# Optimization experiments

Measured on AMD Instinct MI355X. Metric: run time of the kernel, lower is better.

The kernel has to match this reference:

```python
import jax, jax.numpy as jnp
import numpy as np

ALPHA = 0.1

def grad_f(p):
    # analytic gradient of f(p) = sum(p**2)
    return 2.0 * p

def setup_inputs() -> dict:
    key = jax.random.key(0)
    p = jax.random.normal(key, (16384, 64), dtype=jnp.float32)
    return {"p": p}

def reference(p):
    # p: [N, D]
    g = grad_f(p)                                   # [N, D]
    scores = jnp.einsum('id,jd->ij', g, g)          # torch.inner(g, g) -> [N, N]
    w = jax.nn.softmax(-scores, axis=-1)            # [N, N]
    # einsum('ijd,ij->id', p[None,:,:]-p[:,None,:], w)
    #   = w @ p - sum_j(w[i,j]) * p[i]   (avoids the NxNxD intermediate)
    agg = jnp.matmul(w, p) - jnp.sum(w, axis=-1, keepdims=True) * p  # [N, D]
    return p + agg * ALPHA
```

## Files before the change

kernel.cpp:

```cpp
#include <hip/hip_runtime.h>
#include <stdint.h>

#define NROWS 16384
#define DIM 64
#define BK 64
#define NT (NROWS / BK)
#define NQB (NROWS / 128)
#define TILE_BYTES 16384
#define VT_OFF 8192
#define LOG2E 1.4426950408889634f
#define MHAT_COEF 20.0f

typedef __attribute__((ext_vector_type(8))) _Float16 f16x8;
typedef __attribute__((ext_vector_type(8))) unsigned short ushort8;
typedef __attribute__((ext_vector_type(4))) float f32x4;
typedef __attribute__((ext_vector_type(8))) __bf16 bf16x8;
typedef __attribute__((ext_vector_type(8))) short short8;

static __device__ __forceinline__ f32x4 mfma_f16(f16x8 a, f16x8 b, f32x4 c) {
  return __builtin_amdgcn_mfma_f32_16x16x32_f16(a, b, c, 0, 0, 0);
}
static __device__ __forceinline__ f32x4 mfma_bf16(short8 a, short8 b, f32x4 c) {
  return __builtin_amdgcn_mfma_f32_16x16x32_bf16(
      __builtin_bit_cast(bf16x8, a), __builtin_bit_cast(bf16x8, b), c, 0, 0, 0);
}
static __device__ __forceinline__ void gload_lds16(const void* g, void* l) {
  __builtin_amdgcn_global_load_lds(
      (const __attribute__((address_space(1))) unsigned int*)(uintptr_t)g,
      (__attribute__((address_space(3))) unsigned int*)(unsigned int)(uintptr_t)l,
      16, 0, 0);
}
static __device__ __forceinline__ float fast_exp2(float x) {
  return __builtin_amdgcn_exp2f(x);
}
static __device__ __forceinline__ unsigned short f2bfbits(float x) {
  return __builtin_bit_cast(unsigned short, (__bf16)x);
}
static __device__ __forceinline__ unsigned short f2bf(float x) {
  unsigned u = __builtin_bit_cast(unsigned, x);
  u = (u + 0x7fffu + ((u >> 16) & 1u)) >> 16;
  return (unsigned short)u;
}
static __device__ __forceinline__ float bf2f(unsigned short b) {
  return __builtin_bit_cast(float, ((unsigned)b) << 16);
}

__global__ __launch_bounds__(256)
void pack_kernel(const float* __restrict__ p, unsigned char* __restrict__ tiles,
                 float* __restrict__ mhat) {
  __shared__ unsigned short sT[64][68];
  const int kt = blockIdx.x;
  const int t  = threadIdx.x;
  const int r  = t >> 2;
  const int q4 = t & 3;
  const int d0 = q4 * 16;

  const float* src = p + ((size_t)(kt * 64 + r)) * DIM + d0;
  float4 f0 = ((const float4*)src)[0];
  float4 f1 = ((const float4*)src)[1];
  float4 f2 = ((const float4*)src)[2];
  float4 f3 = ((const float4*)src)[3];
  float v[16] = {f0.x, f0.y, f0.z, f0.w, f1.x, f1.y, f1.z, f1.w,
                 f2.x, f2.y, f2.z, f2.w, f3.x, f3.y, f3.z, f3.w};
  ushort8 h0, h1, hb0, hb1;
  float sq = 0.f;
#pragma unroll
  for (int i = 0; i < 8; ++i) {
    h0[i]  = __builtin_bit_cast(unsigned short, (_Float16)v[i]);
    h1[i]  = __builtin_bit_cast(unsigned short, (_Float16)v[8 + i]);
    hb0[i] = f2bf(v[i]);
    hb1[i] = f2bf(v[8 + i]);
    sq = fmaf(v[i], v[i], sq);
    sq = fmaf(v[8 + i], v[8 + i], sq);
  }
  unsigned char* tb = tiles + (size_t)kt * TILE_BYTES;
  const int swz = (r & 7) << 4;
  *(ushort8*)(tb + r * 128 + ((2 * d0) ^ swz))      = h0;
  *(ushort8*)(tb + r * 128 + ((2 * d0 + 16) ^ swz)) = h1;

  sq += __shfl_xor(sq, 1);
  sq += __shfl_xor(sq, 2);
  if (q4 == 0) mhat[kt * 64 + r] = MHAT_COEF * LOG2E * sqrtf(sq);

  *(ushort8*)&sT[r][d0]     = hb0;
  *(ushort8*)&sT[r][d0 + 8] = hb1;
  __syncthreads();
  const int d    = t >> 2;
  const int base = (q4 >> 1) * 32 + (q4 & 1) * 8;
  ushort8 a8, b8;
#pragma unroll
  for (int j = 0; j < 8; ++j) {
    a8[j] = sT[base + (j >> 2) * 16 + (j & 3)][d];
    b8[j] = sT[base + (j >> 2) * 16 + 4 + (j & 3)][d];
  }
  const int swzd = (d & 7) << 4;
  *(ushort8*)(tb + VT_OFF + d * 128 + ((2 * (q4 * 16)) ^ swzd))      = a8;
  *(ushort8*)(tb + VT_OFF + d * 128 + ((2 * (q4 * 16) + 16) ^ swzd)) = b8;
}

__global__ __launch_bounds__(256)
void attn_main(const float* __restrict__ p, const unsigned char* __restrict__ tiles,
               const float* __restrict__ mhat, float* __restrict__ out,
               float* __restrict__ partO, float* __restrict__ partL,
               int S, int writeDirect) {
  __shared__ __align__(16) unsigned char sbuf[2][TILE_BYTES];

  const int t  = threadIdx.x;
  const int w  = t >> 6;
  const int l  = t & 63;
  const int lr = l & 15;
  const int lg = l >> 4;
  const int qt = blockIdx.x;
  const int s  = blockIdx.y;
  const int ntp = NT / S;
  const int kt0 = s * ntp;
  const int swz = (lr & 7) << 4;
  const int ko0 = (lg * 16) ^ swz;
  const int ko1 = (64 + lg * 16) ^ swz;

  f16x8 qf[2][2];
  float nm[2];
#pragma unroll
  for (int g = 0; g < 2; ++g) {
    const int grow = w * 32 + g * 16;
    const unsigned char* qtb =
        tiles + (size_t)(qt * 2 + (grow >> 6)) * TILE_BYTES;
    const int rin = (grow & 63) + lr;
    qf[g][0] = *(const f16x8*)(qtb + rin * 128 + ko0);
    qf[g][1] = *(const f16x8*)(qtb + rin * 128 + ko1);
    nm[g] = -mhat[qt * 128 + grow + lr];
  }

  const f32x4 z4 = {0.f, 0.f, 0.f, 0.f};
  f32x4 oacc[2][4] = {{z4, z4, z4, z4}, {z4, z4, z4, z4}};
  float lrun[2] = {0.f, 0.f};
  const float S2 = -4.0f * LOG2E;

  auto STAGE = [&](int kt, int b) {
    const unsigned char* g = tiles + (size_t)kt * TILE_BYTES + (w * 4) * 1024 + l * 16;
    unsigned char* lb = &sbuf[b][(w * 4) * 1024];
#pragma unroll
    for (int c = 0; c < 4; ++c)
      gload_lds16(g + c * 1024, lb + c * 1024);
  };

  STAGE(kt0, 0);
  __syncthreads();

  for (int i = 0; i < ntp; ++i) {
    if (i + 1 < ntp) STAGE(kt0 + i + 1, (i + 1) & 1);

    const unsigned char* kb = &sbuf[i & 1][0];

    f32x4 acc[2][4] = {{z4, z4, z4, z4}, {z4, z4, z4, z4}};
#pragma unroll
    for (int c = 0; c < 4; ++c) {
      f16x8 kf0 = *(const f16x8*)(kb + (c * 16 + lr) * 128 + ko0);
      f16x8 kf1 = *(const f16x8*)(kb + (c * 16 + lr) * 128 + ko1);
      acc[0][c] = mfma_f16(kf0, qf[0][0], acc[0][c]);
      acc[1][c] = mfma_f16(kf0, qf[1][0], acc[1][c]);
      acc[0][c] = mfma_f16(kf1, qf[0][1], acc[0][c]);
      acc[1][c] = mfma_f16(kf1, qf[1][1], acc[1][c]);
    }

    short8 pb[2][2];
#pragma unroll
    for (int g = 0; g < 2; ++g) {
      float pe[4][4];
#pragma unroll
      for (int c = 0; c < 4; ++c) {
#pragma unroll
        for (int r = 0; r < 4; ++r)
          pe[c][r] = fast_exp2(fmaf(acc[g][c][r], S2, nm[g]));
        lrun[g] += (pe[c][0] + pe[c][1]) + (pe[c][2] + pe[c][3]);
      }
#pragma unroll
      for (int r = 0; r < 4; ++r) {
        pb[g][0][r]     = (short)f2bfbits(pe[0][r]);
        pb[g][0][4 + r] = (short)f2bfbits(pe[1][r]);
        pb[g][1][r]     = (short)f2bfbits(pe[2][r]);
        pb[g][1][4 + r] = (short)f2bfbits(pe[3][r]);
      }
    }

#pragma unroll
    for (int kc = 0; kc < 2; ++kc) {
      const int ko = kc ? ko1 : ko0;
#pragma unroll
      for (int dc = 0; dc < 4; ++dc) {
        short8 vb = *(const short8*)(kb + VT_OFF + (dc * 16 + lr) * 128 + ko);
        oacc[0][dc] = mfma_bf16(pb[0][kc], vb, oacc[0][dc]);
        oacc[1][dc] = mfma_bf16(pb[1][kc], vb, oacc[1][dc]);
      }
    }

    __syncthreads();
  }

#pragma unroll
  for (int g = 0; g < 2; ++g) {
    float lsum = lrun[g];
    lsum += __shfl_xor(lsum, 16);
    lsum += __shfl_xor(lsum, 32);

    if (writeDirect) {
      float lq[4];
#pragma unroll
      for (int r = 0; r < 4; ++r) lq[r] = __shfl(lsum, lg * 4 + r);
#pragma unroll
      for (int r = 0; r < 4; ++r) {
        const float inv = 1.0f / lq[r];
        const size_t grow = (size_t)(qt * 128 + w * 32 + g * 16 + lg * 4 + r) * DIM;
#pragma unroll
        for (int dc = 0; dc < 4; ++dc) {
          const int col = dc * 16 + lr;
          const float pv = p[grow + col];
          out[grow + col] = pv + 0.1f * (oacc[g][dc][r] * inv - pv);
        }
      }
    } else {
      float* po = partO + (size_t)(qt * S + s) * 8192;
      float* pl = partL + (size_t)(qt * S + s) * 128;
#pragma unroll
      for (int r = 0; r < 4; ++r) {
        const int row = w * 32 + g * 16 + lg * 4 + r;
#pragma unroll
        for (int dc = 0; dc < 4; ++dc)
          po[row * 64 + dc * 16 + lr] = oacc[g][dc][r];
      }
      if (l < 16) pl[w * 32 + g * 16 + l] = lsum;
    }
  }
}

__global__ __launch_bounds__(256)
void reduce_kernel(const float* __restrict__ p, const float* __restrict__ partO,
                   const float* __restrict__ partL, float* __restrict__ out, int S) {
  const int t   = threadIdx.x;
  const int row = blockIdx.x * 16 + (t >> 4);
  const int c0  = (t & 15) * 4;
  const int qt  = row >> 7;
  const int rin = row & 127;

  float L = 0.f;
  float4 O = {0.f, 0.f, 0.f, 0.f};
  for (int s2 = 0; s2 < S; ++s2) {
    const size_t b = (size_t)(qt * S + s2);
    L += partL[b * 128 + rin];
    const float4 o4 = *(const float4*)&partO[b * 8192 + rin * 64 + c0];
    O.x += o4.x; O.y += o4.y; O.z += o4.z; O.w += o4.w;
  }
  const float inv = 1.0f / L;
  const float4 pv = *(const float4*)&p[(size_t)row * DIM + c0];
  float4 r;
  r.x = pv.x + 0.1f * (O.x * inv - pv.x);
  r.y = pv.y + 0.1f * (O.y * inv - pv.y);
  r.z = pv.z + 0.1f * (O.z * inv - pv.z);
  r.w = pv.w + 0.1f * (O.w * inv - pv.w);
  *(float4*)&out[(size_t)row * DIM + c0] = r;
}

#define LDE 88
__global__ __launch_bounds__(256)
void grad_attn_fb(const float* __restrict__ p, float* __restrict__ out) {
  __shared__ __align__(16) unsigned short sKhi[BK][LDE];
  __shared__ __align__(16) unsigned short sKlo[BK][LDE];
  __shared__ __align__(16) unsigned short sVt[DIM][LDE];
  __shared__ __align__(16) unsigned short sP[4][16][LDE];
  const int t = threadIdx.x, w = t >> 6, l = t & 63, lr = l & 15, lg = l >> 4;
  const int q0 = blockIdx.x * 64 + w * 16;
  short8 qhi[2], qlo[2];
#pragma unroll
  for (int kc = 0; kc < 2; ++kc) {
    const float* qp = p + (size_t)(q0 + lr) * DIM + kc * 32 + lg * 8;
    float4 fa = *(const float4*)qp;
    float4 fb = *(const float4*)(qp + 4);
    float v[8] = {fa.x, fa.y, fa.z, fa.w, fb.x, fb.y, fb.z, fb.w};
    short8 h, lo2;
#pragma unroll
    for (int i = 0; i < 8; ++i) {
      unsigned short hb = f2bf(v[i]);
      h[i] = (short)hb;
      lo2[i] = (short)f2bf(v[i] - bf2f(hb));
    }
    qhi[kc] = h; qlo[kc] = lo2;
  }
  const f32x4 z4 = {0.f, 0.f, 0.f, 0.f};
  f32x4 oacc[4] = {z4, z4, z4, z4};
  float mrun[4] = {-1e30f, -1e30f, -1e30f, -1e30f};
  float lrun[4] = {0.f, 0.f, 0.f, 0.f};
  const int srow = (t >> 3) * 2, sc0 = (t & 7) * 8;
  const int scs = sc0 ^ (((srow >> 3) & 7) << 3);
  const float S2 = -4.0f * LOG2E;
  for (int kt = 0; kt < NT; ++kt) {
    const int kv0 = kt * BK;
    __syncthreads();
    {
      const float* s0 = p + (size_t)(kv0 + srow) * DIM + sc0;
      float4 a0 = *(const float4*)s0;
      float4 b0 = *(const float4*)(s0 + 4);
      float4 a1 = *(const float4*)(s0 + DIM);
      float4 b1 = *(const float4*)(s0 + DIM + 4);
      float v0[8] = {a0.x, a0.y, a0.z, a0.w, b0.x, b0.y, b0.z, b0.w};
      float v1[8] = {a1.x, a1.y, a1.z, a1.w, b1.x, b1.y, b1.z, b1.w};
      short8 h0, h1, l0, l1;
#pragma unroll
      for (int i = 0; i < 8; ++i) {
        unsigned short hb0 = f2bf(v0[i]);
        unsigned short hb1 = f2bf(v1[i]);
        h0[i] = (short)hb0; l0[i] = (short)f2bf(v0[i] - bf2f(hb0));
        h1[i] = (short)hb1; l1[i] = (short)f2bf(v1[i] - bf2f(hb1));
      }
      *(short8*)&sKhi[srow][scs] = h0;
      *(short8*)&sKlo[srow][scs] = l0;
      *(short8*)&sKhi[srow + 1][scs] = h1;
      *(short8*)&sKlo[srow + 1][scs] = l1;
#pragma unroll
      for (int i = 0; i < 8; ++i) {
        int d = sc0 + i;
        unsigned pk = (unsigned)(unsigned short)h0[i] |
                      (((unsigned)(unsigned short)h1[i]) << 16);
        *(unsigned*)&sVt[d][srow ^ (((d >> 3) & 7) << 3)] = pk;
      }
    }
    __syncthreads();
    f32x4 acc[4] = {z4, z4, z4, z4};
#pragma unroll
    for (int c = 0; c < 4; ++c) {
      const int krow = c * 16 + lr;
      const int swc = ((krow >> 3) & 7) << 3;
#pragma unroll
      for (int kc = 0; kc < 2; ++kc) {
        const int off = (kc * 32 + lg * 8) ^ swc;
        short8 bh = *(const short8*)&sKhi[krow][off];
        short8 bl = *(const short8*)&sKlo[krow][off];
        acc[c] = mfma_bf16(qhi[kc], bh, acc[c]);
        acc[c] = mfma_bf16(qhi[kc], bl, acc[c]);
        acc[c] = mfma_bf16(qlo[kc], bh, acc[c]);
      }
    }
    float P[4][4];
#pragma unroll
    for (int r = 0; r < 4; ++r) {
      float e0 = acc[0][r] * S2, e1 = acc[1][r] * S2;
      float e2 = acc[2][r] * S2, e3 = acc[3][r] * S2;
      float mt = fmaxf(fmaxf(e0, e1), fmaxf(e2, e3));
      mt = fmaxf(mt, __shfl_xor(mt, 1));
      mt = fmaxf(mt, __shfl_xor(mt, 2));
      mt = fmaxf(mt, __shfl_xor(mt, 4));
      mt = fmaxf(mt, __shfl_xor(mt, 8));
      const float mn = fmaxf(mrun[r], mt);
      const float sc = exp2f(mrun[r] - mn);
      mrun[r] = mn;
      float p0 = exp2f(e0 - mn), p1 = exp2f(e1 - mn);
      float p2 = exp2f(e2 - mn), p3 = exp2f(e3 - mn);
      P[0][r] = p0; P[1][r] = p1; P[2][r] = p2; P[3][r] = p3;
      float ps = (p0 + p1) + (p2 + p3);
      ps += __shfl_xor(ps, 1);
      ps += __shfl_xor(ps, 2);
      ps += __shfl_xor(ps, 4);
      ps += __shfl_xor(ps, 8);
      lrun[r] = lrun[r] * sc + ps;
#pragma unroll
      for (int dc = 0; dc < 4; ++dc) oacc[dc][r] *= sc;
    }
    {
      const int irow = lg * 4;
      const int swp = ((l >> 5) & 1) << 3;
#pragma unroll
      for (int c = 0; c < 4; ++c) {
        const int colb = (c * 16 + lr) ^ swp;
#pragma unroll
        for (int r = 0; r < 4; ++r) sP[w][irow + r][colb] = f2bf(P[c][r]);
      }
    }
#pragma unroll
    for (int kc = 0; kc < 2; ++kc) {
      const int kb = kc * 32 + lg * 8;
      short8 pa = *(const short8*)&sP[w][lr][kb ^ (((lr >> 3) & 1) << 3)];
#pragma unroll
      for (int dc = 0; dc < 4; ++dc) {
        const int d = dc * 16 + lr;
        short8 vb = *(const short8*)&sVt[d][kb ^ (((d >> 3) & 7) << 3)];
        oacc[dc] = mfma_bf16(pa, vb, oacc[dc]);
      }
    }
  }
#pragma unroll
  for (int r = 0; r < 4; ++r) {
    const float inv = 1.0f / lrun[r];
    const size_t grow = (size_t)(q0 + lg * 4 + r) * DIM;
#pragma unroll
    for (int dc = 0; dc < 4; ++dc) {
      const int col = dc * 16 + lr;
      const float pv = p[grow + col];
      out[grow + col] = pv + 0.1f * (oacc[dc][r] * inv - pv);
    }
  }
}

extern "C" void kernel_launch(void* const* d_in, const int* in_sizes, int n_in,
                              void* d_out, int out_size, void* d_ws, size_t ws_size,
                              hipStream_t stream) {
  const float* p = (const float*)d_in[0];
  float* out = (float*)d_out;
  unsigned char* ws = (unsigned char*)d_ws;
  const size_t tiles_bytes = (size_t)NT * TILE_BYTES;
  const size_t mhat_bytes  = (size_t)NROWS * sizeof(float);
  const size_t base = tiles_bytes + mhat_bytes;

  if (ws_size < base) {
    grad_attn_fb<<<dim3(NROWS / 64), dim3(256), 0, stream>>>(p, out);
    return;
  }
  int S = 16;
  while (S > 1) {
    size_t need = base + (size_t)NQB * S * (8192 + 128) * sizeof(float);
    if (need <= ws_size) break;
    S >>= 1;
  }
  float* mhat  = (float*)(ws + tiles_bytes);
  float* partO = (float*)(ws + base);
  float* partL = partO + (size_t)NQB * S * 8192;

  pack_kernel<<<dim3(NT), dim3(256), 0, stream>>>(p, ws, mhat);
  attn_main<<<dim3(NQB, S), dim3(256), 0, stream>>>(p, ws, mhat, out, partO, partL,
                                                    S, S == 1 ? 1 : 0);
  if (S > 1)
    reduce_kernel<<<dim3(NROWS / 16), dim3(256), 0, stream>>>(p, partO, partL, out, S);
}
```

Baseline: 97.40 us.

## Split waves across query and key halves with LDS cross-wave reduction

The four waves are repartitioned from 4 query groups of 32 rows into 2 query groups of 64 rows times 2 key halves. Each wave now holds 64 query rows and processes 32 keys per tile. K and V fragments loaded from LDS are therefore reused across 4 query sub-blocks instead of 2, which halves LDS fragment reads per MFMA. At the end the two key-half waves combine their output accumulators and row sums through shared memory before the epilogue. This costs more registers (oacc grows to 4x4) and adds an extra sync plus an LDS reduction, and only half the waves do the final writes.

```diff
diff --git a/kernel.cpp b/kernel.cpp
--- a/kernel.cpp
+++ b/kernel.cpp
@@ -104,36 +104,42 @@
                float* __restrict__ partO, float* __restrict__ partL,
                int S, int writeDirect) {
   __shared__ __align__(16) unsigned char sbuf[2][TILE_BYTES];
-
-  const int t  = threadIdx.x;
-  const int w  = t >> 6;
-  const int l  = t & 63;
-  const int lr = l & 15;
-  const int lg = l >> 4;
-  const int qt = blockIdx.x;
-  const int s  = blockIdx.y;
+  __shared__ float sL[2][4][64];
+
+  const int t   = threadIdx.x;
+  const int w   = t >> 6;
+  const int l   = t & 63;
+  const int lr  = l & 15;
+  const int lg  = l >> 4;
+  const int wq  = w >> 1;
+  const int wkv = w & 1;
+  const int qt  = blockIdx.x;
+  const int s   = blockIdx.y;
   const int ntp = NT / S;
   const int kt0 = s * ntp;
   const int swz = (lr & 7) << 4;
   const int ko0 = (lg * 16) ^ swz;
   const int ko1 = (64 + lg * 16) ^ swz;
-
-  f16x8 qf[2][2];
-  float nm[2];
-#pragma unroll
-  for (int g = 0; g < 2; ++g) {
-    const int grow = w * 32 + g * 16;
-    const unsigned char* qtb =
-        tiles + (size_t)(qt * 2 + (grow >> 6)) * TILE_BYTES;
-    const int rin = (grow & 63) + lr;
+  const int kopv = (wkv * 64 + lg * 16) ^ swz;
+
+  const unsigned char* qtb = tiles + (size_t)(qt * 2 + wq) * TILE_BYTES;
+  f16x8 qf[4][2];
+  float nm[4];
+#pragma unroll
+  for (int g = 0; g < 4; ++g) {
+    const int rin = g * 16 + lr;
     qf[g][0] = *(const f16x8*)(qtb + rin * 128 + ko0);
     qf[g][1] = *(const f16x8*)(qtb + rin * 128 + ko1);
-    nm[g] = -mhat[qt * 128 + grow + lr];
+    nm[g] = -mhat[qt * 128 + wq * 64 + g * 16 + lr];
   }
 
   const f32x4 z4 = {0.f, 0.f, 0.f, 0.f};
-  f32x4 oacc[2][4] = {{z4, z4, z4, z4}, {z4, z4, z4, z4}};
-  float lrun[2] = {0.f, 0.f};
+  f32x4 oacc[4][4];
+#pragma unroll
+  for (int g = 0; g < 4; ++g)
+#pragma unroll
+    for (int dc = 0; dc < 4; ++dc) oacc[g][dc] = z4;
+  float lrun[4] = {0.f, 0.f, 0.f, 0.f};
   const float S2 = -4.0f * LOG2E;
 
   auto STAGE = [&](int kt, int b) {
@@ -152,83 +158,107 @@
 
     const unsigned char* kb = &sbuf[i & 1][0];
 
-    f32x4 acc[2][4] = {{z4, z4, z4, z4}, {z4, z4, z4, z4}};
-#pragma unroll
-    for (int c = 0; c < 4; ++c) {
-      f16x8 kf0 = *(const f16x8*)(kb + (c * 16 + lr) * 128 + ko0);
-      f16x8 kf1 = *(const f16x8*)(kb + (c * 16 + lr) * 128 + ko1);
-      acc[0][c] = mfma_f16(kf0, qf[0][0], acc[0][c]);
-      acc[1][c] = mfma_f16(kf0, qf[1][0], acc[1][c]);
-      acc[0][c] = mfma_f16(kf1, qf[0][1], acc[0][c]);
-      acc[1][c] = mfma_f16(kf1, qf[1][1], acc[1][c]);
-    }
-
-    short8 pb[2][2];
-#pragma unroll
-    for (int g = 0; g < 2; ++g) {
-      float pe[4][4];
-#pragma unroll
-      for (int c = 0; c < 4; ++c) {
-#pragma unroll
-        for (int r = 0; r < 4; ++r)
-          pe[c][r] = fast_exp2(fmaf(acc[g][c][r], S2, nm[g]));
-        lrun[g] += (pe[c][0] + pe[c][1]) + (pe[c][2] + pe[c][3]);
-      }
+    f32x4 acc[4][2];
+#pragma unroll
+    for (int g = 0; g < 4; ++g) { acc[g][0] = z4; acc[g][1] = z4; }
+#pragma unroll
+    for (int c = 0; c < 2; ++c) {
+      const int krow = (wkv * 32 + c * 16 + lr) * 128;
+      f16x8 kf0 = *(const f16x8*)(kb + krow + ko0);
+      f16x8 kf1 = *(const f16x8*)(kb + krow + ko1);
+#pragma unroll
+      for (int g = 0; g < 4; ++g) {
+        acc[g][c] = mfma_f16(kf0, qf[g][0], acc[g][c]);
+        acc[g][c] = mfma_f16(kf1, qf[g][1], acc[g][c]);
+      }
+    }
+
+    short8 pb[4];
+#pragma unroll
+    for (int g = 0; g < 4; ++g) {
+      f32x4 pe0, pe1;
 #pragma unroll
       for (int r = 0; r < 4; ++r) {
-        pb[g][0][r]     = (short)f2bfbits(pe[0][r]);
-        pb[g][0][4 + r] = (short)f2bfbits(pe[1][r]);
-        pb[g][1][r]     = (short)f2bfbits(pe[2][r]);
-        pb[g][1][4 + r] = (short)f2bfbits(pe[3][r]);
-      }
-    }
-
-#pragma unroll
-    for (int kc = 0; kc < 2; ++kc) {
-      const int ko = kc ? ko1 : ko0;
+        pe0[r] = fast_exp2(fmaf(acc[g][0][r], S2, nm[g]));
+        pe1[r] = fast_exp2(fmaf(acc[g][1][r], S2, nm[g]));
+      }
+      lrun[g] += (pe0[0] + pe0[1]) + (pe0[2] + pe0[3]) +
+                 (pe1[0] + pe1[1]) + (pe1[2] + pe1[3]);
+#pragma unroll
+      for (int r = 0; r < 4; ++r) {
+        pb[g][r]     = (short)f2bfbits(pe0[r]);
+        pb[g][4 + r] = (short)f2bfbits(pe1[r]);
+      }
+    }
+
+#pragma unroll
+    for (int dc = 0; dc < 4; ++dc) {
+      short8 vb = *(const short8*)(kb + VT_OFF + (dc * 16 + lr) * 128 + kopv);
+#pragma unroll
+      for (int g = 0; g < 4; ++g)
+        oacc[g][dc] = mfma_bf16(pb[g], vb, oacc[g][dc]);
+    }
+
+    __syncthreads();
+  }
+
+  if (wkv == 1) {
+    unsigned char* xb = &sbuf[0][0] + wq * 16384;
+#pragma unroll
+    for (int g = 0; g < 4; ++g) {
+#pragma unroll
+      for (int dc = 0; dc < 4; ++dc)
+        *(f32x4*)(xb + (((g * 4 + dc) * 64) + l) * 16) = oacc[g][dc];
+      sL[wq][g][l] = lrun[g];
+    }
+  }
+  __syncthreads();
+  if (wkv == 0) {
+    const unsigned char* xb = &sbuf[0][0] + wq * 16384;
+#pragma unroll
+    for (int g = 0; g < 4; ++g) {
 #pragma unroll
       for (int dc = 0; dc < 4; ++dc) {
-        short8 vb = *(const short8*)(kb + VT_OFF + (dc * 16 + lr) * 128 + ko);
-        oacc[0][dc] = mfma_bf16(pb[0][kc], vb, oacc[0][dc]);
-        oacc[1][dc] = mfma_bf16(pb[1][kc], vb, oacc[1][dc]);
-      }
-    }
-
-    __syncthreads();
-  }
-
-#pragma unroll
-  for (int g = 0; g < 2; ++g) {
-    float lsum = lrun[g];
-    lsum += __shfl_xor(lsum, 16);
-    lsum += __shfl_xor(lsum, 32);
-
-    if (writeDirect) {
-      float lq[4];
-#pragma unroll
-      for (int r = 0; r < 4; ++r) lq[r] = __shfl(lsum, lg * 4 + r);
-#pragma unroll
-      for (int r = 0; r < 4; ++r) {
-        const float inv = 1.0f / lq[r];
-        const size_t grow = (size_t)(qt * 128 + w * 32 + g * 16 + lg * 4 + r) * DIM;
-#pragma unroll
-        for (int dc = 0; dc < 4; ++dc) {
-          const int col = dc * 16 + lr;
-          const float pv = p[grow + col];
-          out[grow + col] = pv + 0.1f * (oacc[g][dc][r] * inv - pv);
+        f32x4 o2 = *(const f32x4*)(xb + (((g * 4 + dc) * 64) + l) * 16);
+        oacc[g][dc] += o2;
+      }
+      lrun[g] += sL[wq][g][l];
+    }
+
+#pragma unroll
+    for (int g = 0; g < 4; ++g) {
+      float lsum = lrun[g];
+      lsum += __shfl_xor(lsum, 16);
+      lsum += __shfl_xor(lsum, 32);
+
+      if (writeDirect) {
+        float lq[4];
+#pragma unroll
+        for (int r = 0; r < 4; ++r) lq[r] = __shfl(lsum, lg * 4 + r);
+#pragma unroll
+        for (int r = 0; r < 4; ++r) {
+          const float inv = 1.0f / lq[r];
+          const size_t grow =
+              (size_t)(qt * 128 + wq * 64 + g * 16 + lg * 4 + r) * DIM;
+#pragma unroll
+          for (int dc = 0; dc < 4; ++dc) {
+            const int col = dc * 16 + lr;
+            const float pv = p[grow + col];
+            out[grow + col] = pv + 0.1f * (oacc[g][dc][r] * inv - pv);
+          }
         }
-      }
-    } else {
-      float* po = partO + (size_t)(qt * S + s) * 8192;
-      float* pl = partL + (size_t)(qt * S + s) * 128;
-#pragma unroll
-      for (int r = 0; r < 4; ++r) {
-        const int row = w * 32 + g * 16 + lg * 4 + r;
-#pragma unroll
-        for (int dc = 0; dc < 4; ++dc)
-          po[row * 64 + dc * 16 + lr] = oacc[g][dc][r];
-      }
-      if (l < 16) pl[w * 32 + g * 16 + l] = lsum;
+      } else {
+        float* po = partO + (size_t)(qt * S + s) * 8192;
+        float* pl = partL + (size_t)(qt * S + s) * 128;
+#pragma unroll
+        for (int r = 0; r < 4; ++r) {
+          const int row = wq * 64 + g * 16 + lg * 4 + r;
+#pragma unroll
+          for (int dc = 0; dc < 4; ++dc)
+            po[row * 64 + dc * 16 + lr] = oacc[g][dc][r];
+        }
+        if (l < 16) pl[wq * 64 + g * 16 + l] = lsum;
+      }
     }
   }
 }
```

Measured after the change: 112.0 us. 15.0% more time.
